# Performance work log

Measured on AMD Instinct MI355X. Metric: run time of the kernel, lower is better.

The kernel has to match this reference:

```python
import jax, jax.numpy as jnp
import numpy as np

NN_SIZE = 10


def batch_normals(x, k=NN_SIZE):
    """x: (B, 3, N) NCHW point cloud -> per-point normals (B, 3, N).

    kNN (including self) -> local covariance -> smallest eigenvector.
    """
    pts = jnp.transpose(x, (0, 2, 1))  # (B, N, 3)
    sq = jnp.sum(pts * pts, axis=-1)  # (B, N)
    # pairwise squared distances (B, N, N); the inner product is a big GEMM
    d2 = sq[:, :, None] + sq[:, None, :] - 2.0 * jnp.einsum('bnd,bmd->bnm', pts, pts)
    _, idx = jax.lax.top_k(-d2, k)  # (B, N, k) nearest neighbors (incl. self)
    nbrs = jax.vmap(lambda p, i: p[i])(pts, idx)  # (B, N, k, 3)
    centered = nbrs - jnp.mean(nbrs, axis=2, keepdims=True)
    cov = jnp.einsum('bnki,bnkj->bnij', centered, centered) / k  # (B, N, 3, 3)
    _, vecs = jnp.linalg.eigh(cov)  # eigenvalues ascending
    normal = vecs[..., :, 0]  # eigenvector of smallest eigenvalue, (B, N, 3)
    return jnp.transpose(normal, (0, 2, 1))  # (B, 3, N)


def setup_inputs() -> dict:
    key = jax.random.key(0)
    k1, k2 = jax.random.split(key)
    pred = jax.random.normal(k1, (8, 3, 4096), dtype=jnp.float32)
    gt = jax.random.normal(k2, (8, 3, 4096), dtype=jnp.float32)
    return {"pred": pred, "gt": gt}


def reference(pred, gt):
    pred_normals = batch_normals(pred)
    gt_normals = batch_normals(gt)
    # metric = "mse"
    return jnp.mean((pred_normals - gt_normals) ** 2)
```

## Files before the change

kernel.cpp:

```cpp
#include <hip/hip_runtime.h>
#include <math.h>

#define NPTS 4096
#define KNN 10
#define CAP 48
#define TAU_SLACK 1e-4f
#define NRM_N (8 * 3 * NPTS)
#define DYN_BYTES (NPTS * 16 + 128 * CAP * 2 + 512)

__device__ __forceinline__ float med3f(float a, float b, float c) {
    return __builtin_amdgcn_fmed3f(a, b, c);
}


__device__ __forceinline__ float slapy2_(float x, float y) {
    float ax = fabsf(x), ay = fabsf(y);
    float w = fmaxf(ax, ay), z = fminf(ax, ay);
    if (z == 0.f) return w;
    float t = z / w;
    return w * sqrtf(1.f + t * t);
}

__device__ __forceinline__ void slartg_(float f, float g, float* c, float* s, float* r) {
    if (g == 0.f) { *c = 1.f; *s = 0.f; *r = f; }
    else if (f == 0.f) { *c = 0.f; *s = copysignf(1.f, g); *r = fabsf(g); }
    else {
        float f1 = fabsf(f);
        float d = sqrtf(f * f + g * g);
        float rr = copysignf(d, f);
        *c = f1 / d;
        *s = g / rr;
        *r = rr;
    }
}

__device__ void slaev2_(float a, float b, float c,
                        float* rt1, float* rt2, float* cs1, float* sn1) {
    float sm = a + c;
    float df = a - c;
    float adf = fabsf(df);
    float tb = b + b;
    float ab = fabsf(tb);
    float acmx, acmn;
    if (fabsf(a) > fabsf(c)) { acmx = a; acmn = c; } else { acmx = c; acmn = a; }
    float rt;
    if (adf > ab)      { float t = ab / adf; rt = adf * sqrtf(1.f + t * t); }
    else if (adf < ab) { float t = adf / ab; rt = ab * sqrtf(1.f + t * t); }
    else               { rt = ab * sqrtf(2.f); }
    int sgn1;
    if (sm < 0.f) {
        *rt1 = 0.5f * (sm - rt); sgn1 = -1;
        *rt2 = (acmx / *rt1) * acmn - (b / *rt1) * b;
    } else if (sm > 0.f) {
        *rt1 = 0.5f * (sm + rt); sgn1 = 1;
        *rt2 = (acmx / *rt1) * acmn - (b / *rt1) * b;
    } else {
        *rt1 = 0.5f * rt; *rt2 = -0.5f * rt; sgn1 = 1;
    }
    int sgn2;
    float cs;
    if (df >= 0.f) { cs = df + rt; sgn2 = 1; } else { cs = df - rt; sgn2 = -1; }
    float acs = fabsf(cs);
    if (acs > ab) {
        float ct = -tb / cs;
        *sn1 = 1.f / sqrtf(1.f + ct * ct);
        *cs1 = ct * (*sn1);
    } else {
        if (ab == 0.f) { *cs1 = 1.f; *sn1 = 0.f; }
        else {
            float tn = -cs / tb;
            *cs1 = 1.f / sqrtf(1.f + tn * tn);
            *sn1 = tn * (*cs1);
        }
    }
    if (sgn1 == sgn2) { float tn = *cs1; *cs1 = -(*sn1); *sn1 = tn; }
}

__device__ void steqr3_(float* d, float* e, float Z[3][3]) {
    const float eps    = 5.9604644775390625e-8f;
    const float eps2   = eps * eps;
    const float safmin = 1.17549435e-38f;
    const int n = 3, nm1 = 2;
    const int nmaxit = 90;
    int jtot = 0, l1 = 1;
    int guard = 0;

    while (l1 <= n) {
        if (++guard > 600) break;
        if (l1 > 1) e[l1 - 2] = 0.f;
        int m = n;
        if (l1 <= nm1) {
            for (int mm = l1; mm <= nm1; ++mm) {
                float tst = fabsf(e[mm - 1]);
                if (tst == 0.f) { m = mm; break; }
                if (tst <= (sqrtf(fabsf(d[mm - 1])) * sqrtf(fabsf(d[mm]))) * eps) {
                    e[mm - 1] = 0.f; m = mm; break;
                }
            }
        }
        int l = l1, lsv = l1, lend = m, lendsv = m;
        l1 = m + 1;
        if (lend == l) continue;
        float anorm = 0.f;
        for (int i = l; i <= lend; i++) anorm = fmaxf(anorm, fabsf(d[i - 1]));
        for (int i = l; i <= lend - 1; i++) anorm = fmaxf(anorm, fabsf(e[i - 1]));
        if (anorm == 0.f) continue;
        if (fabsf(d[lend - 1]) < fabsf(d[l - 1])) { lend = lsv; l = lendsv; }

        if (lend > l) {
            for (;;) {
                if (++guard > 600) return;
                int m2 = lend;
                if (l != lend) {
                    for (int mm = l; mm <= lend - 1; ++mm) {
                        float tst = e[mm - 1] * e[mm - 1];
                        if (tst <= (eps2 * fabsf(d[mm - 1])) * fabsf(d[mm]) + safmin) { m2 = mm; break; }
                    }
                }
                if (m2 < lend) e[m2 - 1] = 0.f;
                float p = d[l - 1];
                if (m2 == l) {
                    d[l - 1] = p; l = l + 1;
                    if (l <= lend) continue;
                    break;
                }
                if (m2 == l + 1) {
                    float rt1, rt2, c, s;
                    slaev2_(d[l - 1], e[l - 1], d[l], &rt1, &rt2, &c, &s);
                    for (int i = 0; i < 3; i++) {
                        float t = Z[i][l];
                        Z[i][l]     = c * t - s * Z[i][l - 1];
                        Z[i][l - 1] = s * t + c * Z[i][l - 1];
                    }
                    d[l - 1] = rt1; d[l] = rt2; e[l - 1] = 0.f;
                    l += 2;
                    if (l <= lend) continue;
                    break;
                }
                if (jtot == nmaxit) break;
                jtot++;
                float g = (d[l] - p) / (2.f * e[l - 1]);
                float r = slapy2_(g, 1.f);
                g = d[m2 - 1] - p + e[l - 1] / (g + copysignf(r, g));
                float s = 1.f, c = 1.f;
                p = 0.f;
                float csv[2], snv[2];
                for (int i = m2 - 1; i >= l; --i) {
                    float f = s * e[i - 1];
                    float b = c * e[i - 1];
                    slartg_(g, f, &c, &s, &r);
                    if (i != m2 - 1) e[i] = r;
                    g = d[i] - p;
                    r = (d[i - 1] - g) * s + 2.f * c * b;
                    p = s * r;
                    d[i] = g + p;
                    g = c * r - b;
                    csv[i - l] = c; snv[i - l] = -s;
                }
                int nrot = m2 - l;
                for (int j = nrot; j >= 1; --j) {
                    float C = csv[j - 1], S = snv[j - 1];
                    for (int i = 0; i < 3; i++) {
                        float t = Z[i][l - 1 + j];
                        Z[i][l - 1 + j] = C * t - S * Z[i][l - 2 + j];
                        Z[i][l - 2 + j] = S * t + C * Z[i][l - 2 + j];
                    }
                }
                d[l - 1] = d[l - 1] - p;
                e[l - 1] = g;
            }
        } else {
            for (;;) {
                if (++guard > 600) return;
                int m2 = lend;
                if (l != lend) {
                    for (int mm = l; mm >= lend + 1; --mm) {
                        float tst = e[mm - 2] * e[mm - 2];
                        if (tst <= (eps2 * fabsf(d[mm - 1])) * fabsf(d[mm - 2]) + safmin) { m2 = mm; break; }
                    }
                }
                if (m2 > lend) e[m2 - 2] = 0.f;
                float p = d[l - 1];
                if (m2 == l) {
                    d[l - 1] = p; l = l - 1;
                    if (l >= lend) continue;
                    break;
                }
                if (m2 == l - 1) {
                    float rt1, rt2, c, s;
                    slaev2_(d[l - 2], e[l - 2], d[l - 1], &rt1, &rt2, &c, &s);
                    for (int i = 0; i < 3; i++) {
                        float t = Z[i][l - 1];
                        Z[i][l - 1] = c * t - s * Z[i][l - 2];
                        Z[i][l - 2] = s * t + c * Z[i][l - 2];
                    }
                    d[l - 2] = rt1; d[l - 1] = rt2; e[l - 2] = 0.f;
                    l -= 2;
                    if (l >= lend) continue;
                    break;
                }
                if (jtot == nmaxit) break;
                jtot++;
                float g = (d[l - 2] - p) / (2.f * e[l - 2]);
                float r = slapy2_(g, 1.f);
                g = d[m2 - 1] - p + e[l - 2] / (g + copysignf(r, g));
                float s = 1.f, c = 1.f;
                p = 0.f;
                float csv[2], snv[2];
                for (int i = m2; i <= l - 1; ++i) {
                    float f = s * e[i - 1];
                    float b = c * e[i - 1];
                    slartg_(g, f, &c, &s, &r);
                    if (i != m2) e[i - 2] = r;
                    g = d[i - 1] - p;
                    r = (d[i] - g) * s + 2.f * c * b;
                    p = s * r;
                    d[i - 1] = g + p;
                    g = c * r - b;
                    csv[i - m2] = c; snv[i - m2] = s;
                }
                int nrot = l - m2;
                for (int j = 1; j <= nrot; ++j) {
                    float C = csv[j - 1], S = snv[j - 1];
                    for (int i = 0; i < 3; i++) {
                        float t = Z[i][m2 - 1 + j];
                        Z[i][m2 - 1 + j] = C * t - S * Z[i][m2 - 2 + j];
                        Z[i][m2 - 2 + j] = S * t + C * Z[i][m2 - 2 + j];
                    }
                }
                d[l - 1] -= p;
                e[l - 2] = g;
            }
        }
    }
    for (int ii = 2; ii <= n; ++ii) {
        int i = ii - 1, k = i;
        float p = d[i - 1];
        for (int j = ii; j <= n; ++j) {
            if (d[j - 1] < p) { k = j; p = d[j - 1]; }
        }
        if (k != i) {
            d[k - 1] = d[i - 1]; d[i - 1] = p;
            for (int r2 = 0; r2 < 3; r2++) {
                float t = Z[r2][i - 1]; Z[r2][i - 1] = Z[r2][k - 1]; Z[r2][k - 1] = t;
            }
        }
    }
}

__device__ void eig_normal3(const float xs[KNN], const float ys[KNN], const float zs[KNN],
                            float out[3]) {
    float mx = 0.f, my = 0.f, mz = 0.f;
#pragma unroll
    for (int s = 0; s < KNN; s++) { mx += xs[s]; my += ys[s]; mz += zs[s]; }
    mx /= 10.0f; my /= 10.0f; mz /= 10.0f;

    float c00 = 0.f, c10 = 0.f, c20 = 0.f, c11 = 0.f, c21 = 0.f, c22 = 0.f;
#pragma unroll
    for (int s = 0; s < KNN; s++) {
        float dx = xs[s] - mx, dy = ys[s] - my, dz = zs[s] - mz;
        c00 = fmaf(dx, dx, c00);
        c10 = fmaf(dy, dx, c10);
        c20 = fmaf(dz, dx, c20);
        c11 = fmaf(dy, dy, c11);
        c21 = fmaf(dz, dy, c21);
        c22 = fmaf(dz, dz, c22);
    }
    c00 /= 10.0f; c10 /= 10.0f; c20 /= 10.0f; c11 /= 10.0f; c21 /= 10.0f; c22 /= 10.0f;

    float alpha = c10, x2 = c20;
    float tau, v2, beta;
    float xnorm = fabsf(x2);
    if (xnorm == 0.f) { tau = 0.f; v2 = 0.f; beta = alpha; }
    else {
        beta = -copysignf(slapy2_(alpha, xnorm), alpha);
        tau = (beta - alpha) / beta;
        v2 = x2 / (alpha - beta);
    }
    float d[3], e[2];
    d[0] = c00;
    if (tau != 0.f) {
        float p0 = tau * (c11 + c21 * v2);
        float p1 = tau * (c21 + c22 * v2);
        float aw = -0.5f * tau * (p0 + p1 * v2);
        float w0 = p0 + aw;
        float w1 = p1 + aw * v2;
        d[1] = (c11 - w0) - w0;
        e[1] = (c21 - v2 * w0) - w1;
        d[2] = (c22 - v2 * w1) - w1 * v2;
        e[0] = beta;
    } else {
        d[1] = c11; d[2] = c22; e[0] = beta; e[1] = c21;
    }

    float Z[3][3] = {{1.f, 0.f, 0.f}, {0.f, 1.f, 0.f}, {0.f, 0.f, 1.f}};
    steqr3_(d, e, Z);

    float y0 = Z[0][0], y1 = Z[1][0], y2 = Z[2][0];
    if (tau != 0.f) {
        float t = tau * (y1 + v2 * y2);
        y1 = y1 - t;
        y2 = y2 - t * v2;
    }
    out[0] = y0; out[1] = y1; out[2] = y2;
}

__device__ __forceinline__ void merge_round(float* v, int off) {
    float t[KNN];
#pragma unroll
    for (int i = 0; i < KNN; i++) t[i] = fminf(v[i], __shfl_xor(v[KNN - 1 - i], off));
#define CE(a, b) { float hi = fmaxf(t[a], t[b]); float lo = fminf(t[a], t[b]); t[a] = hi; t[b] = lo; }
    CE(0, 8) CE(1, 9)
    CE(0, 4) CE(1, 5) CE(2, 6) CE(3, 7)
    CE(0, 2) CE(1, 3) CE(4, 6) CE(5, 7)
    CE(0, 1) CE(2, 3) CE(4, 5) CE(6, 7) CE(8, 9)
#undef CE
#pragma unroll
    for (int i = 0; i < KNN; i++) v[i] = t[i];
}

__device__ void do_phase4(const float* __restrict__ src, int chunk, int tid,
                          float4* pts, unsigned short* spairs, int* scnt,
                          float nv[3]) {
    for (int j = tid; j < NPTS; j += 512) {
        float x = src[j], y = src[NPTS + j], z = src[2 * NPTS + j];
        float w = fmaf(z, z, fmaf(y, y, x * x));
        pts[j] = make_float4(x, y, z, w);
    }
    if (tid < 128) scnt[tid] = 0;
    __syncthreads();

    int part = tid & 15;
    int qg = tid >> 4;
    int ql0 = qg * 4;
    int q0 = chunk * 128 + ql0;

    float m2x[4], m2y[4], m2z[4];
#pragma unroll
    for (int c = 0; c < 4; c++) {
        float4 p = pts[q0 + c];
        m2x[c] = -2.f * p.x; m2y[c] = -2.f * p.y; m2z[c] = -2.f * p.z;
    }

    float v[4][KNN + 1];
#pragma unroll
    for (int c = 0; c < 4; c++) {
#pragma unroll
        for (int s = 0; s < KNN; s++) v[c][s] = INFINITY;
        v[c][KNN] = -INFINITY;
    }

#pragma unroll 2
    for (int g = 0; g < 32; g++) {
        int jb = part + 128 * g;
        float m[4] = {INFINITY, INFINITY, INFINITY, INFINITY};
#pragma unroll
        for (int u = 0; u < 8; u++) {
            float4 p = pts[jb + 16 * u];
#pragma unroll
            for (int c = 0; c < 4; c++) {
                float key = fmaf(m2z[c], p.z, fmaf(m2y[c], p.y, fmaf(m2x[c], p.x, p.w)));
                m[c] = fminf(m[c], key);
            }
        }
#pragma unroll
        for (int c = 0; c < 4; c++)
#pragma unroll
            for (int s = 0; s < KNN; s++) v[c][s] = med3f(m[c], v[c][s], v[c][s + 1]);
    }

    float tauS[4];
#pragma unroll
    for (int c = 0; c < 4; c++) {
        merge_round(v[c], 1);
        merge_round(v[c], 2);
        merge_round(v[c], 4);
        merge_round(v[c], 8);
        tauS[c] = v[c][0] + TAU_SLACK;
    }

#pragma unroll 2
    for (int mm = 0; mm < 256; mm++) {
        int j = part + 16 * mm;
        float4 p = pts[j];
#pragma unroll
        for (int c = 0; c < 4; c++) {
            float key = fmaf(m2z[c], p.z, fmaf(m2y[c], p.y, fmaf(m2x[c], p.x, p.w)));
            if (key <= tauS[c]) {
                int ql = ql0 + c;
                int pos = atomicAdd(&scnt[ql], 1);
                if (pos < CAP) spairs[ql * CAP + pos] = (unsigned short)j;
            }
        }
    }
    __syncthreads();

    if (tid < 128) {
        int ql = tid;
        int qi = chunk * 128 + ql;
        float4 q = pts[qi];
        float qw = q.w;
        int cnt = scnt[ql];

        float bd[KNN]; int bi_[KNN];
#pragma unroll
        for (int s = 0; s < KNN; s++) { bd[s] = 3.4e38f; bi_[s] = 0; }
        float worst = 3.4e38f;
        int wslot = 0;
        if (cnt > CAP) {
            for (int j = 0; j < NPTS; j++) {
                float4 p = pts[j];
                float dot = fmaf(q.z, p.z, fmaf(q.y, p.y, q.x * p.x));
                float d2 = (qw + p.w) - 2.f * dot;
                if (d2 < worst) {
#pragma unroll
                    for (int s = 0; s < KNN; s++) { if (s == wslot) { bd[s] = d2; bi_[s] = j; } }
                    float wm = bd[0]; int ws = 0;
#pragma unroll
                    for (int s = 1; s < KNN; s++) { if (bd[s] > wm) { wm = bd[s]; ws = s; } }
                    worst = wm; wslot = ws;
                }
            }
        } else {
            for (int t = 0; t < cnt; t++) {
                int j = spairs[ql * CAP + t];
                float4 p = pts[j];
                float dot = fmaf(q.z, p.z, fmaf(q.y, p.y, q.x * p.x));
                float d2 = (qw + p.w) - 2.f * dot;
                if (d2 < worst) {
#pragma unroll
                    for (int s = 0; s < KNN; s++) { if (s == wslot) { bd[s] = d2; bi_[s] = j; } }
                    float wm = bd[0]; int ws = 0;
#pragma unroll
                    for (int s = 1; s < KNN; s++) { if (bd[s] > wm) { wm = bd[s]; ws = s; } }
                    worst = wm; wslot = ws;
                }
            }
        }
#pragma unroll
        for (int a = 0; a < KNN - 1; a++)
#pragma unroll
            for (int b2 = 0; b2 < KNN - 1 - a; b2++) {
                bool sw = (bd[b2] > bd[b2 + 1]) ||
                          (bd[b2] == bd[b2 + 1] && bi_[b2] > bi_[b2 + 1]);
                float d_lo = sw ? bd[b2 + 1] : bd[b2];
                float d_hi = sw ? bd[b2] : bd[b2 + 1];
                int   i_lo = sw ? bi_[b2 + 1] : bi_[b2];
                int   i_hi = sw ? bi_[b2] : bi_[b2 + 1];
                bd[b2] = d_lo; bd[b2 + 1] = d_hi; bi_[b2] = i_lo; bi_[b2 + 1] = i_hi;
            }
        float xs[KNN], ys[KNN], zs[KNN];
#pragma unroll
        for (int s = 0; s < KNN; s++) {
            float4 p = pts[bi_[s]];
            xs[s] = p.x; ys[s] = p.y; zs[s] = p.z;
        }
        eig_normal3(xs, ys, zs, nv);
    }
    __syncthreads();
}

__global__ __launch_bounds__(512, 4) void normals4_kernel(const float* __restrict__ pred,
                                                          const float* __restrict__ gt,
                                                          float* __restrict__ nrm,
                                                          float* __restrict__ out) {
    extern __shared__ char dynlds[];
    float4* pts = (float4*)dynlds;
    unsigned short* spairs = (unsigned short*)(dynlds + NPTS * 16);
    int* scnt = (int*)(dynlds + NPTS * 16 + 128 * CAP * 2);

    int tid = threadIdx.x;
    int bid = blockIdx.x;
    if (bid == 0 && tid == 0) out[0] = 0.f;
    int cloud = bid >> 8;
    int b = (bid >> 5) & 7;
    int chunk = bid & 31;

    const float* src = (cloud == 0 ? pred : gt) + (size_t)b * 3 * NPTS;
    float nv[3] = {0.f, 0.f, 0.f};
    do_phase4(src, chunk, tid, pts, spairs, scnt, nv);

    if (tid < 128) {
        int qg2 = chunk * 128 + tid;
        float* dst = nrm + ((size_t)cloud * 8 + b) * 3 * NPTS;
        dst[0 * NPTS + qg2] = nv[0];
        dst[1 * NPTS + qg2] = nv[1];
        dst[2 * NPTS + qg2] = nv[2];
    }
}

__device__ void do_phase_static(const float* __restrict__ src, int chunk, int tid,
                                float2* sxy, float* sz, unsigned short* spairs, int* scnt,
                                float nv[3]) {
    for (int j = tid; j < NPTS; j += 512) {
        float x = src[j], y = src[NPTS + j], z = src[2 * NPTS + j];
        sxy[j] = make_float2(x, y);
        sz[j] = z;
    }
    if (tid < 128) scnt[tid] = 0;
    __syncthreads();

    int part = tid & 15;
    int qg = tid >> 4;
    int ql0 = qg * 4;
    int q0 = chunk * 128 + ql0;

    float m2x[4], m2y[4], m2z[4];
#pragma unroll
    for (int c = 0; c < 4; c++) {
        float2 a = sxy[q0 + c];
        float z = sz[q0 + c];
        m2x[c] = -2.f * a.x; m2y[c] = -2.f * a.y; m2z[c] = -2.f * z;
    }

    float v[4][KNN + 1];
#pragma unroll
    for (int c = 0; c < 4; c++) {
#pragma unroll
        for (int s = 0; s < KNN; s++) v[c][s] = INFINITY;
        v[c][KNN] = -INFINITY;
    }

#pragma unroll 2
    for (int g = 0; g < 32; g++) {
        int jb = part + 128 * g;
        float m[4] = {INFINITY, INFINITY, INFINITY, INFINITY};
#pragma unroll
        for (int u = 0; u < 8; u++) {
            int j = jb + 16 * u;
            float2 a = sxy[j];
            float z = sz[j];
            float w = fmaf(z, z, fmaf(a.y, a.y, a.x * a.x));
#pragma unroll
            for (int c = 0; c < 4; c++) {
                float key = fmaf(m2z[c], z, fmaf(m2y[c], a.y, fmaf(m2x[c], a.x, w)));
                m[c] = fminf(m[c], key);
            }
        }
#pragma unroll
        for (int c = 0; c < 4; c++)
#pragma unroll
            for (int s = 0; s < KNN; s++) v[c][s] = med3f(m[c], v[c][s], v[c][s + 1]);
    }

    float tauS[4];
#pragma unroll
    for (int c = 0; c < 4; c++) {
        merge_round(v[c], 1);
        merge_round(v[c], 2);
        merge_round(v[c], 4);
        merge_round(v[c], 8);
        tauS[c] = v[c][0] + TAU_SLACK;
    }

#pragma unroll 2
    for (int mm = 0; mm < 256; mm++) {
        int j = part + 16 * mm;
        float2 a = sxy[j];
        float z = sz[j];
        float w = fmaf(z, z, fmaf(a.y, a.y, a.x * a.x));
#pragma unroll
        for (int c = 0; c < 4; c++) {
            float key = fmaf(m2z[c], z, fmaf(m2y[c], a.y, fmaf(m2x[c], a.x, w)));
            if (key <= tauS[c]) {
                int ql = ql0 + c;
                int pos = atomicAdd(&scnt[ql], 1);
                if (pos < CAP) spairs[ql * CAP + pos] = (unsigned short)j;
            }
        }
    }
    __syncthreads();

    if (tid < 128) {
        int ql = tid;
        int qi = chunk * 128 + ql;
        float2 qa = sxy[qi];
        float qzz = sz[qi];
        float qw = fmaf(qzz, qzz, fmaf(qa.y, qa.y, qa.x * qa.x));
        int cnt = scnt[ql];

        float bd[KNN]; int bi_[KNN];
#pragma unroll
        for (int s = 0; s < KNN; s++) { bd[s] = 3.4e38f; bi_[s] = 0; }
        float worst = 3.4e38f;
        int wslot = 0;
        if (cnt > CAP) {
            for (int j = 0; j < NPTS; j++) {
                float2 a = sxy[j];
                float z = sz[j];
                float w = fmaf(z, z, fmaf(a.y, a.y, a.x * a.x));
                float dot = fmaf(qzz, z, fmaf(qa.y, a.y, qa.x * a.x));
                float d2 = (qw + w) - 2.f * dot;
                if (d2 < worst) {
#pragma unroll
                    for (int s = 0; s < KNN; s++) { if (s == wslot) { bd[s] = d2; bi_[s] = j; } }
                    float wm = bd[0]; int ws = 0;
#pragma unroll
                    for (int s = 1; s < KNN; s++) { if (bd[s] > wm) { wm = bd[s]; ws = s; } }
                    worst = wm; wslot = ws;
                }
            }
        } else {
            for (int t = 0; t < cnt; t++) {
                int j = spairs[ql * CAP + t];
                float2 a = sxy[j];
                float z = sz[j];
                float w = fmaf(z, z, fmaf(a.y, a.y, a.x * a.x));
                float dot = fmaf(qzz, z, fmaf(qa.y, a.y, qa.x * a.x));
                float d2 = (qw + w) - 2.f * dot;
                if (d2 < worst) {
#pragma unroll
                    for (int s = 0; s < KNN; s++) { if (s == wslot) { bd[s] = d2; bi_[s] = j; } }
                    float wm = bd[0]; int ws = 0;
#pragma unroll
                    for (int s = 1; s < KNN; s++) { if (bd[s] > wm) { wm = bd[s]; ws = s; } }
                    worst = wm; wslot = ws;
                }
            }
        }
#pragma unroll
        for (int a = 0; a < KNN - 1; a++)
#pragma unroll
            for (int b2 = 0; b2 < KNN - 1 - a; b2++) {
                bool sw = (bd[b2] > bd[b2 + 1]) ||
                          (bd[b2] == bd[b2 + 1] && bi_[b2] > bi_[b2 + 1]);
                float d_lo = sw ? bd[b2 + 1] : bd[b2];
                float d_hi = sw ? bd[b2] : bd[b2 + 1];
                int   i_lo = sw ? bi_[b2 + 1] : bi_[b2];
                int   i_hi = sw ? bi_[b2] : bi_[b2 + 1];
                bd[b2] = d_lo; bd[b2 + 1] = d_hi; bi_[b2] = i_lo; bi_[b2 + 1] = i_hi;
            }
        float xs[KNN], ys[KNN], zs[KNN];
#pragma unroll
        for (int s = 0; s < KNN; s++) {
            int j = bi_[s];
            float2 a = sxy[j];
            xs[s] = a.x; ys[s] = a.y; zs[s] = sz[j];
        }
        eig_normal3(xs, ys, zs, nv);
    }
    __syncthreads();
}

__global__ __launch_bounds__(512, 4) void normals_kernel(const float* __restrict__ pred,
                                                         const float* __restrict__ gt,
                                                         float* __restrict__ nrm,
                                                         float* __restrict__ out) {
    __shared__ float2 sxy[NPTS];
    __shared__ float  sz[NPTS];
    __shared__ unsigned short spairs[128 * CAP];
    __shared__ int scnt[128];

    int tid = threadIdx.x;
    int bid = blockIdx.x;
    if (bid == 0 && tid == 0) out[0] = 0.f;
    int cloud = bid >> 8;
    int b = (bid >> 5) & 7;
    int chunk = bid & 31;

    const float* src = (cloud == 0 ? pred : gt) + (size_t)b * 3 * NPTS;
    float nv[3] = {0.f, 0.f, 0.f};
    do_phase_static(src, chunk, tid, sxy, sz, spairs, scnt, nv);

    if (tid < 128) {
        int qg2 = chunk * 128 + tid;
        float* dst = nrm + ((size_t)cloud * 8 + b) * 3 * NPTS;
        dst[0 * NPTS + qg2] = nv[0];
        dst[1 * NPTS + qg2] = nv[1];
        dst[2 * NPTS + qg2] = nv[2];
    }
}

__global__ __launch_bounds__(256) void loss_kernel(const float* __restrict__ nrm,
                                                   float* __restrict__ out) {
    const int n = NRM_N;
    const float* a = nrm;
    const float* b = nrm + n;
    float acc = 0.f;
    for (int i = blockIdx.x * 256 + threadIdx.x; i < n; i += gridDim.x * 256) {
        float dd = a[i] - b[i];
        acc = fmaf(dd, dd, acc);
    }
#pragma unroll
    for (int off = 32; off > 0; off >>= 1) acc += __shfl_down(acc, off);
    __shared__ float wsum[4];
    int lane = threadIdx.x & 63, wv = threadIdx.x >> 6;
    if (lane == 0) wsum[wv] = acc;
    __syncthreads();
    if (threadIdx.x == 0) {
        float t = wsum[0] + wsum[1] + wsum[2] + wsum[3];
        atomicAdd(out, t * (1.f / (float)n));
    }
}

extern "C" void kernel_launch(void* const* d_in, const int* in_sizes, int n_in,
                              void* d_out, int out_size, void* d_ws, size_t ws_size,
                              hipStream_t stream) {
    (void)in_sizes; (void)n_in; (void)out_size;
    const float* pred = (const float*)d_in[0];
    const float* gt   = (const float*)d_in[1];
    float* out = (float*)d_out;

    size_t need = (size_t)2 * NRM_N * sizeof(float);
    float* nrm = (float*)d_ws;

    int dev = 0;
    hipGetDevice(&dev);
    int maxShm = 0;
    hipDeviceGetAttribute(&maxShm, hipDeviceAttributeMaxSharedMemoryPerBlock, dev);
    hipError_t eAttr = hipFuncSetAttribute(
        reinterpret_cast<const void*>(normals4_kernel),
        hipFuncAttributeMaxDynamicSharedMemorySize, DYN_BYTES);
    bool use4 = (ws_size >= need) && ((maxShm >= DYN_BYTES) || (eAttr == hipSuccess));

    if (use4) {
        hipLaunchKernelGGL(normals4_kernel, dim3(512), dim3(512), DYN_BYTES, stream,
                           pred, gt, nrm, out);
        hipLaunchKernelGGL(loss_kernel, dim3(96), dim3(256), 0, stream, nrm, out);
    } else {
        hipLaunchKernelGGL(normals_kernel, dim3(512), dim3(512), 0, stream,
                           pred, gt, nrm, out);
        hipLaunchKernelGGL(loss_kernel, dim3(96), dim3(256), 0, stream, nrm, out);
    }
}
```

Measured before the change: 168.3 us.

## Split kNN and eigen-solve into separate kernels with chunked LDS staging

Replaces the single fused normals kernel with a kNN index kernel and a separate eigenvector kernel. The kNN kernel handles 64 queries per block (1024 blocks instead of 512) and streams the point cloud through a 16 KB LDS tile in 1 KB-point chunks, so LDS use drops and more blocks can be resident. The eigen solve now runs one thread per query across all threads rather than only 128 of 512 threads per block. The cost is reloading and re-staging points twice per block from global memory, writing and reading a neighbour-index buffer, reading coordinates from global in the refine step, and one extra kernel launch.

Result: no change. 169.1 us (+0.5%).

```diff
diff --git a/kernel.cpp b/kernel.cpp
--- a/kernel.cpp
+++ b/kernel.cpp
@@ -6,7 +6,9 @@
 #define CAP 48
 #define TAU_SLACK 1e-4f
 #define NRM_N (8 * 3 * NPTS)
-#define DYN_BYTES (NPTS * 16 + 128 * CAP * 2 + 512)
+#define QPB 64
+#define CHUNK 1024
+#define NCH (NPTS / CHUNK)
 
 __device__ __forceinline__ float med3f(float a, float b, float c) {
     return __builtin_amdgcn_fmed3f(a, b, c);
@@ -319,59 +321,77 @@
     for (int i = 0; i < KNN; i++) v[i] = t[i];
 }
 
-__device__ void do_phase4(const float* __restrict__ src, int chunk, int tid,
-                          float4* pts, unsigned short* spairs, int* scnt,
-                          float nv[3]) {
-    for (int j = tid; j < NPTS; j += 512) {
-        float x = src[j], y = src[NPTS + j], z = src[2 * NPTS + j];
-        float w = fmaf(z, z, fmaf(y, y, x * x));
-        pts[j] = make_float4(x, y, z, w);
-    }
-    if (tid < 128) scnt[tid] = 0;
-    __syncthreads();
+__global__ __launch_bounds__(512, 8) void knn_idx_kernel(const float* __restrict__ pred,
+                                                         const float* __restrict__ gt,
+                                                         unsigned short* __restrict__ idxout,
+                                                         float* __restrict__ out) {
+    __shared__ float4 pts[CHUNK];
+    __shared__ unsigned short spairs[QPB * CAP];
+    __shared__ int scnt[QPB];
+
+    int tid = threadIdx.x;
+    int bid = blockIdx.x;
+    if (bid == 0 && tid == 0) out[0] = 0.f;
+    int cloud = bid >> 9;
+    int b = (bid >> 6) & 7;
+    int chunkq = bid & 63;
+
+    const float* src = (cloud == 0 ? pred : gt) + (size_t)b * 3 * NPTS;
 
     int part = tid & 15;
     int qg = tid >> 4;
-    int ql0 = qg * 4;
-    int q0 = chunk * 128 + ql0;
-
-    float m2x[4], m2y[4], m2z[4];
-#pragma unroll
-    for (int c = 0; c < 4; c++) {
-        float4 p = pts[q0 + c];
-        m2x[c] = -2.f * p.x; m2y[c] = -2.f * p.y; m2z[c] = -2.f * p.z;
-    }
-
-    float v[4][KNN + 1];
-#pragma unroll
-    for (int c = 0; c < 4; c++) {
+    int ql0 = qg * 2;
+    int q0 = chunkq * QPB + ql0;
+
+    if (tid < QPB) scnt[tid] = 0;
+
+    float m2x[2], m2y[2], m2z[2];
+#pragma unroll
+    for (int c = 0; c < 2; c++) {
+        float x = src[q0 + c], y = src[NPTS + q0 + c], z = src[2 * NPTS + q0 + c];
+        m2x[c] = -2.f * x; m2y[c] = -2.f * y; m2z[c] = -2.f * z;
+    }
+
+    float v[2][KNN + 1];
+#pragma unroll
+    for (int c = 0; c < 2; c++) {
 #pragma unroll
         for (int s = 0; s < KNN; s++) v[c][s] = INFINITY;
         v[c][KNN] = -INFINITY;
     }
 
+    for (int h = 0; h < NCH; h++) {
+        if (h) __syncthreads();
+        for (int j2 = tid; j2 < CHUNK; j2 += 512) {
+            int j = h * CHUNK + j2;
+            float x = src[j], y = src[NPTS + j], z = src[2 * NPTS + j];
+            float w = fmaf(z, z, fmaf(y, y, x * x));
+            pts[j2] = make_float4(x, y, z, w);
+        }
+        __syncthreads();
 #pragma unroll 2
-    for (int g = 0; g < 32; g++) {
-        int jb = part + 128 * g;
-        float m[4] = {INFINITY, INFINITY, INFINITY, INFINITY};
-#pragma unroll
-        for (int u = 0; u < 8; u++) {
-            float4 p = pts[jb + 16 * u];
-#pragma unroll
-            for (int c = 0; c < 4; c++) {
-                float key = fmaf(m2z[c], p.z, fmaf(m2y[c], p.y, fmaf(m2x[c], p.x, p.w)));
-                m[c] = fminf(m[c], key);
-            }
-        }
-#pragma unroll
-        for (int c = 0; c < 4; c++)
-#pragma unroll
-            for (int s = 0; s < KNN; s++) v[c][s] = med3f(m[c], v[c][s], v[c][s + 1]);
-    }
-
-    float tauS[4];
-#pragma unroll
-    for (int c = 0; c < 4; c++) {
+        for (int g2 = 0; g2 < 8; g2++) {
+            int jb = part + 128 * g2;
+            float m[2] = {INFINITY, INFINITY};
+#pragma unroll
+            for (int u = 0; u < 8; u++) {
+                float4 p = pts[jb + 16 * u];
+#pragma unroll
+                for (int c = 0; c < 2; c++) {
+                    float key = fmaf(m2z[c], p.z, fmaf(m2y[c], p.y, fmaf(m2x[c], p.x, p.w)));
+                    m[c] = fminf(m[c], key);
+                }
+            }
+#pragma unroll
+            for (int c = 0; c < 2; c++)
+#pragma unroll
+                for (int s = 0; s < KNN; s++) v[c][s] = med3f(m[c], v[c][s], v[c][s + 1]);
+        }
+    }
+
+    float tauS[2];
+#pragma unroll
+    for (int c = 0; c < 2; c++) {
         merge_round(v[c], 1);
         merge_round(v[c], 2);
         merge_round(v[c], 4);
@@ -379,27 +399,37 @@
         tauS[c] = v[c][0] + TAU_SLACK;
     }
 
+    for (int h = 0; h < NCH; h++) {
+        __syncthreads();
+        for (int j2 = tid; j2 < CHUNK; j2 += 512) {
+            int j = h * CHUNK + j2;
+            float x = src[j], y = src[NPTS + j], z = src[2 * NPTS + j];
+            float w = fmaf(z, z, fmaf(y, y, x * x));
+            pts[j2] = make_float4(x, y, z, w);
+        }
+        __syncthreads();
 #pragma unroll 2
-    for (int mm = 0; mm < 256; mm++) {
-        int j = part + 16 * mm;
-        float4 p = pts[j];
-#pragma unroll
-        for (int c = 0; c < 4; c++) {
-            float key = fmaf(m2z[c], p.z, fmaf(m2y[c], p.y, fmaf(m2x[c], p.x, p.w)));
-            if (key <= tauS[c]) {
-                int ql = ql0 + c;
-                int pos = atomicAdd(&scnt[ql], 1);
-                if (pos < CAP) spairs[ql * CAP + pos] = (unsigned short)j;
+        for (int mm = 0; mm < 64; mm++) {
+            int j2 = part + 16 * mm;
+            float4 p = pts[j2];
+#pragma unroll
+            for (int c = 0; c < 2; c++) {
+                float key = fmaf(m2z[c], p.z, fmaf(m2y[c], p.y, fmaf(m2x[c], p.x, p.w)));
+                if (key <= tauS[c]) {
+                    int ql = ql0 + c;
+                    int pos = atomicAdd(&scnt[ql], 1);
+                    if (pos < CAP) spairs[ql * CAP + pos] = (unsigned short)(h * CHUNK + j2);
+                }
             }
         }
     }
     __syncthreads();
 
-    if (tid < 128) {
+    if (tid < QPB) {
         int ql = tid;
-        int qi = chunk * 128 + ql;
-        float4 q = pts[qi];
-        float qw = q.w;
+        int qi = chunkq * QPB + ql;
+        float qx = src[qi], qy = src[NPTS + qi], qz = src[2 * NPTS + qi];
+        float qw = fmaf(qz, qz, fmaf(qy, qy, qx * qx));
         int cnt = scnt[ql];
 
         float bd[KNN]; int bi_[KNN];
@@ -409,9 +439,10 @@
         int wslot = 0;
         if (cnt > CAP) {
             for (int j = 0; j < NPTS; j++) {
-                float4 p = pts[j];
-                float dot = fmaf(q.z, p.z, fmaf(q.y, p.y, q.x * p.x));
-                float d2 = (qw + p.w) - 2.f * dot;
+                float x = src[j], y = src[NPTS + j], z = src[2 * NPTS + j];
+                float w = fmaf(z, z, fmaf(y, y, x * x));
+                float dot = fmaf(qz, z, fmaf(qy, y, qx * x));
+                float d2 = (qw + w) - 2.f * dot;
                 if (d2 < worst) {
 #pragma unroll
                     for (int s = 0; s < KNN; s++) { if (s == wslot) { bd[s] = d2; bi_[s] = j; } }
@@ -424,9 +455,10 @@
         } else {
             for (int t = 0; t < cnt; t++) {
                 int j = spairs[ql * CAP + t];
-                float4 p = pts[j];
-                float dot = fmaf(q.z, p.z, fmaf(q.y, p.y, q.x * p.x));
-                float d2 = (qw + p.w) - 2.f * dot;
+                float x = src[j], y = src[NPTS + j], z = src[2 * NPTS + j];
+                float w = fmaf(z, z, fmaf(y, y, x * x));
+                float dot = fmaf(qz, z, fmaf(qy, y, qx * x));
+                float d2 = (qw + w) - 2.f * dot;
                 if (d2 < worst) {
 #pragma unroll
                     for (int s = 0; s < KNN; s++) { if (s == wslot) { bd[s] = d2; bi_[s] = j; } }
@@ -449,44 +481,37 @@
                 int   i_hi = sw ? bi_[b2] : bi_[b2 + 1];
                 bd[b2] = d_lo; bd[b2 + 1] = d_hi; bi_[b2] = i_lo; bi_[b2 + 1] = i_hi;
             }
-        float xs[KNN], ys[KNN], zs[KNN];
-#pragma unroll
-        for (int s = 0; s < KNN; s++) {
-            float4 p = pts[bi_[s]];
-            xs[s] = p.x; ys[s] = p.y; zs[s] = p.z;
-        }
-        eig_normal3(xs, ys, zs, nv);
-    }
-    __syncthreads();
-}
-
-__global__ __launch_bounds__(512, 4) void normals4_kernel(const float* __restrict__ pred,
-                                                          const float* __restrict__ gt,
-                                                          float* __restrict__ nrm,
-                                                          float* __restrict__ out) {
-    extern __shared__ char dynlds[];
-    float4* pts = (float4*)dynlds;
-    unsigned short* spairs = (unsigned short*)(dynlds + NPTS * 16);
-    int* scnt = (int*)(dynlds + NPTS * 16 + 128 * CAP * 2);
-
-    int tid = threadIdx.x;
-    int bid = blockIdx.x;
-    if (bid == 0 && tid == 0) out[0] = 0.f;
-    int cloud = bid >> 8;
-    int b = (bid >> 5) & 7;
-    int chunk = bid & 31;
-
+        size_t qglobal = ((size_t)cloud * 8 + b) * NPTS + qi;
+#pragma unroll
+        for (int s = 0; s < KNN; s++)
+            idxout[qglobal * KNN + s] = (unsigned short)bi_[s];
+    }
+}
+
+__global__ __launch_bounds__(256) void eig_kernel(const float* __restrict__ pred,
+                                                  const float* __restrict__ gt,
+                                                  const unsigned short* __restrict__ idxin,
+                                                  float* __restrict__ nrm) {
+    int q = blockIdx.x * 256 + threadIdx.x;
+    int cloud = q >> 15;
+    int rem = q & 32767;
+    int b = rem >> 12;
+    int pt = rem & 4095;
     const float* src = (cloud == 0 ? pred : gt) + (size_t)b * 3 * NPTS;
-    float nv[3] = {0.f, 0.f, 0.f};
-    do_phase4(src, chunk, tid, pts, spairs, scnt, nv);
-
-    if (tid < 128) {
-        int qg2 = chunk * 128 + tid;
-        float* dst = nrm + ((size_t)cloud * 8 + b) * 3 * NPTS;
-        dst[0 * NPTS + qg2] = nv[0];
-        dst[1 * NPTS + qg2] = nv[1];
-        dst[2 * NPTS + qg2] = nv[2];
-    }
+
+    float xs[KNN], ys[KNN], zs[KNN];
+#pragma unroll
+    for (int s = 0; s < KNN; s++) {
+        int j = idxin[(size_t)q * KNN + s];
+        xs[s] = src[j]; ys[s] = src[NPTS + j]; zs[s] = src[2 * NPTS + j];
+    }
+    float nv[3];
+    eig_normal3(xs, ys, zs, nv);
+
+    float* dst = nrm + ((size_t)cloud * 8 + b) * 3 * NPTS;
+    dst[0 * NPTS + pt] = nv[0];
+    dst[1 * NPTS + pt] = nv[1];
+    dst[2 * NPTS + pt] = nv[2];
 }
 
 __device__ void do_phase_static(const float* __restrict__ src, int chunk, int tid,
@@ -648,8 +673,8 @@
                                                          float* __restrict__ out) {
     __shared__ float2 sxy[NPTS];
     __shared__ float  sz[NPTS];
-    __shared__ unsigned short spairs[128 * CAP];
-    __shared__ int scnt[128];
+    __shared__ unsigned short spairs_s[128 * CAP];
+    __shared__ int scnt_s[128];
 
     int tid = threadIdx.x;
     int bid = blockIdx.x;
@@ -660,7 +685,7 @@
 
     const float* src = (cloud == 0 ? pred : gt) + (size_t)b * 3 * NPTS;
     float nv[3] = {0.f, 0.f, 0.f};
-    do_phase_static(src, chunk, tid, sxy, sz, spairs, scnt, nv);
+    do_phase_static(src, chunk, tid, sxy, sz, spairs_s, scnt_s, nv);
 
     if (tid < 128) {
         int qg2 = chunk * 128 + tid;
@@ -701,21 +726,16 @@
     const float* gt   = (const float*)d_in[1];
     float* out = (float*)d_out;
 
-    size_t need = (size_t)2 * NRM_N * sizeof(float);
+    size_t need_nrm = (size_t)2 * NRM_N * sizeof(float);
+    size_t need_idx = (size_t)2 * 8 * NPTS * KNN * sizeof(unsigned short);
     float* nrm = (float*)d_ws;
 
-    int dev = 0;
-    hipGetDevice(&dev);
-    int maxShm = 0;
-    hipDeviceGetAttribute(&maxShm, hipDeviceAttributeMaxSharedMemoryPerBlock, dev);
-    hipError_t eAttr = hipFuncSetAttribute(
-        reinterpret_cast<const void*>(normals4_kernel),
-        hipFuncAttributeMaxDynamicSharedMemorySize, DYN_BYTES);
-    bool use4 = (ws_size >= need) && ((maxShm >= DYN_BYTES) || (eAttr == hipSuccess));
-
-    if (use4) {
-        hipLaunchKernelGGL(normals4_kernel, dim3(512), dim3(512), DYN_BYTES, stream,
-                           pred, gt, nrm, out);
+    if (ws_size >= need_nrm + need_idx) {
+        unsigned short* idx = (unsigned short*)((char*)d_ws + need_nrm);
+        hipLaunchKernelGGL(knn_idx_kernel, dim3(1024), dim3(512), 0, stream,
+                           pred, gt, idx, out);
+        hipLaunchKernelGGL(eig_kernel, dim3(256), dim3(256), 0, stream,
+                           pred, gt, idx, nrm);
         hipLaunchKernelGGL(loss_kernel, dim3(96), dim3(256), 0, stream, nrm, out);
     } else {
         hipLaunchKernelGGL(normals_kernel, dim3(512), dim3(512), 0, stream,
```
